# Kernel optimization log

Measured on AMD Instinct MI355X. Metric: run time of the kernel, lower is better.

Reference implementation:

```python
import jax, jax.numpy as jnp
import numpy as np

N_NODES = 100000
N_EDGES = 3200000
N_FEAT = 128
HIDDEN = 16
N_CLASSES = 10
N_GRAPHS = 512


def setup_inputs() -> dict:
    key = jax.random.key(0)
    ks = jax.random.split(key, 12)
    x = jax.random.normal(ks[0], (N_NODES, N_FEAT), dtype=jnp.float32)
    edge_index = jax.random.randint(ks[1], (2, N_EDGES), 0, N_NODES, dtype=jnp.int64)
    batch = jnp.sort(jax.random.randint(ks[2], (N_NODES,), 0, N_GRAPHS, dtype=jnp.int64))
    def glorot(k, fan_in, fan_out):
        s = jnp.sqrt(6.0 / (fan_in + fan_out)).astype(jnp.float32)
        return jax.random.uniform(k, (fan_in, fan_out), jnp.float32, -s, s)
    W1 = glorot(ks[3], N_FEAT, HIDDEN); b1 = jnp.zeros((HIDDEN,), jnp.float32)
    W2 = glorot(ks[4], HIDDEN, HIDDEN); b2 = jnp.zeros((HIDDEN,), jnp.float32)
    W3 = glorot(ks[5], HIDDEN, HIDDEN); b3 = jnp.zeros((HIDDEN,), jnp.float32)
    Wlin = glorot(ks[6], HIDDEN, N_CLASSES)
    blin = jnp.zeros((N_CLASSES,), jnp.float32)
    return {"x": x, "edge_index": edge_index, "batch": batch,
            "W1": W1, "b1": b1, "W2": W2, "b2": b2, "W3": W3, "b3": b3,
            "Wlin": Wlin, "blin": blin}


def _gcn_conv(x, W, b, src, dst, norm, n):
    # h = X W ; out[dst] += norm * h[src] ; + bias
    h = x @ W
    out = jax.ops.segment_sum(h[src] * norm[:, None], dst, num_segments=n)
    return out + b


def reference(x, edge_index, batch, W1, b1, W2, b2, W3, b3, Wlin, blin):
    n = x.shape[0]
    loop = jnp.arange(n, dtype=edge_index.dtype)
    src = jnp.concatenate([edge_index[0], loop])  # add self-loops (PyG GCNConv default)
    dst = jnp.concatenate([edge_index[1], loop])
    # symmetric degree normalization: deg over destination (incl. self-loops)
    deg = jax.ops.segment_sum(jnp.ones_like(dst, dtype=x.dtype), dst, num_segments=n)
    dinv = jnp.where(deg > 0, jax.lax.rsqrt(jnp.maximum(deg, 1.0)), 0.0)
    norm = dinv[src] * dinv[dst]  # [E+N]

    h = jax.nn.relu(_gcn_conv(x, W1, b1, src, dst, norm, n))
    h = jax.nn.relu(_gcn_conv(h, W2, b2, src, dst, norm, n))
    h = _gcn_conv(h, W3, b3, src, dst, norm, n)
    # global add pool over graphs
    pooled = jax.ops.segment_sum(h, batch, num_segments=N_GRAPHS)  # [G, hidden]
    # dropout p=0.5 is identity in eval mode
    return pooled @ Wlin + blin
```

## Files before the change

### kernel.cpp

```cpp
#include <hip/hip_runtime.h>
#include <hip/hip_fp16.h>

#define N_NODES   100000
#define N_EDGES   3200000
#define N_FEAT    128
#define HIDDEN    16
#define N_CLASSES 10
#define N_GRAPHS  512
#define NPB       256
#define NBUCKET   391
#define EPB       4096
#define PBLK      ((N_EDGES + EPB - 1) / EPB)
#define PSLACK    15872
#define CSLACK    9216


__global__ void cursor_init_kernel(int* __restrict__ cur) {
    int i = blockIdx.x * 256 + threadIdx.x;
    if (i < NBUCKET) cur[i] = i * PSLACK;
}

__global__ __launch_bounds__(512) void partition_kernel(const int* __restrict__ src,
                                                        const int* __restrict__ dst,
                                                        int* __restrict__ cur,
                                                        unsigned* __restrict__ part) {
    __shared__ int cnt[NBUCKET];
    __shared__ int lbase[NBUCKET];
    __shared__ int rk[NBUCKET];
    __shared__ int gbase[NBUCKET];
    __shared__ int s[512];
    __shared__ unsigned sorted[EPB];
    __shared__ unsigned short bb[EPB];
    __shared__ unsigned char  dl[EPB];
    int tid = threadIdx.x;
    for (int i = tid; i < NBUCKET; i += 512) cnt[i] = 0;
    __syncthreads();
    int s0 = blockIdx.x * EPB;
#pragma unroll
    for (int i = 0; i < EPB / 512; ++i) {
        int le = i * 512 + tid;
        int e  = s0 + le;
        if (e < N_EDGES) {
            int d = dst[e];
            int b = d >> 8;
            bb[le] = (unsigned short)b;
            dl[le] = (unsigned char)(d & 255);
            atomicAdd(&cnt[b], 1);
        }
    }
    __syncthreads();
    int v = (tid < NBUCKET) ? cnt[tid] : 0;
    s[tid] = v;
    __syncthreads();
    for (int off = 1; off < 512; off <<= 1) {
        int t = (tid >= off) ? s[tid - off] : 0;
        __syncthreads();
        s[tid] += t;
        __syncthreads();
    }
    if (tid < NBUCKET) {
        int lb = s[tid] - v;
        lbase[tid] = lb;
        rk[tid]    = lb;
        int cpad = (v + 15) & ~15;
        gbase[tid] = cpad ? atomicAdd(&cur[tid], cpad) : 0;
    }
    __syncthreads();
#pragma unroll
    for (int i = 0; i < EPB / 512; ++i) {
        int le = i * 512 + tid;
        int e  = s0 + le;
        if (e < N_EDGES) {
            int b = bb[le];
            int r = atomicAdd(&rk[b], 1);
            sorted[r] = (unsigned)src[e] | ((unsigned)dl[le] << 17);
        }
    }
    __syncthreads();
    int w16 = tid >> 4, l16 = tid & 15;
    for (int b = w16; b < NBUCKET; b += 32) {
        int c = cnt[b];
        if (!c) continue;
        int cpad = (c + 15) & ~15;
        int lb = lbase[b], gb = gbase[b];
        for (int j = l16; j < cpad; j += 16)
            part[gb + j] = (j < c) ? sorted[lb + j] : 0xFFFFFFFFu;
    }
}

__global__ __launch_bounds__(512) void build_csr_kernel(const unsigned* __restrict__ part,
                                                        const int* __restrict__ cur,
                                                        int2* __restrict__ rp,
                                                        float* __restrict__ dinv, int* __restrict__ csr) {
    __shared__ int ncnt[256];
    __shared__ int s[512];
    int b   = blockIdx.x;
    int tid = threadIdx.x;
    int beg = b * PSLACK, end = cur[b];
    if (tid < 256) ncnt[tid] = 0;
    __syncthreads();
    for (int j = beg + tid; j < end; j += 512) {
        unsigned r = part[j];
        if (r != 0xFFFFFFFFu) atomicAdd(&ncnt[(r >> 17) & 255], 1);
    }
    __syncthreads();
    int deg = (tid < 256) ? ncnt[tid] : 0;
    s[tid] = deg;
    __syncthreads();
    for (int off = 1; off < 512; off <<= 1) {
        int t = (tid >= off) ? s[tid - off] : 0;
        __syncthreads();
        s[tid] += t;
        __syncthreads();
    }
    int excl = s[tid] - deg;
    int cbeg = b * CSLACK;
    if (tid < 256) {
        int node = b * 256 + tid;
        if (node < N_NODES) {
            rp[node]   = make_int2(cbeg + excl, cbeg + excl + deg);
            dinv[node] = rsqrtf((float)(deg + 1));
        }
    }
    __syncthreads();
    if (tid < 256) ncnt[tid] = cbeg + excl;
    __syncthreads();
    for (int j = beg + tid; j < end; j += 512) {
        unsigned r = part[j];
        if (r != 0xFFFFFFFFu) {
            int vv = (r >> 17) & 255;
            int slot = atomicAdd(&ncnt[vv], 1);
            csr[slot] = (int)(r & 0x1FFFFu);
        }
    }
}


__device__ __forceinline__ void pack_store8(__half* outp, int idx, const float* o) {
    int4 w;
    __half2 q;
    q = __floats2half2_rn(o[0], o[1]); w.x = *(int*)&q;
    q = __floats2half2_rn(o[2], o[3]); w.y = *(int*)&q;
    q = __floats2half2_rn(o[4], o[5]); w.z = *(int*)&q;
    q = __floats2half2_rn(o[6], o[7]); w.w = *(int*)&q;
    ((int4*)outp)[idx] = w;
}

__global__ __launch_bounds__(256) void transform_x_kernel(const float* __restrict__ x,
                                                          const float* __restrict__ W,
                                                          const float* __restrict__ dinv,
                                                          __half* __restrict__ g) {
    __shared__ __half2 Wp[1024];
    int tid = threadIdx.x;
    for (int i = tid; i < 1024; i += 256) {
        int kp = i >> 4, f = i & 15;
        Wp[i] = __floats2half2_rn(W[(2 * kp) * HIDDEN + f], W[(2 * kp + 1) * HIDDEN + f]);
    }
    __syncthreads();
    int l  = tid & 63;
    int wv = tid >> 6;
    int rw = l >> 2;
    int q  = l & 3;
    int row = blockIdx.x * 64 + wv * 16 + rw;
    if (row >= N_NODES) return;
    const float4* xp = (const float4*)x + (size_t)row * 32;
    float4 xr[8];
#pragma unroll
    for (int s8 = 0; s8 < 8; ++s8) xr[s8] = xp[q + 4 * s8];
    __half2 acc[16];
    const __half2 z2 = __floats2half2_rn(0.f, 0.f);
#pragma unroll
    for (int f = 0; f < 16; ++f) acc[f] = z2;
    const int4* w4 = (const int4*)Wp;
#pragma unroll
    for (int s8 = 0; s8 < 8; ++s8) {
        int k4 = q + 4 * s8;
        __half2 xp0 = __floats2half2_rn(xr[s8].x, xr[s8].y);
        __half2 xp1 = __floats2half2_rn(xr[s8].z, xr[s8].w);
#pragma unroll
        for (int hf = 0; hf < 2; ++hf) {
            int kp = 2 * k4 + hf;
            __half2 xv = hf ? xp1 : xp0;
#pragma unroll
            for (int j = 0; j < 4; ++j) {
                int4 wj = w4[kp * 4 + j];
                const __half2* wvv = (const __half2*)&wj;
#pragma unroll
                for (int ff = 0; ff < 4; ++ff)
                    acc[j * 4 + ff] = __hfma2(xv, wvv[ff], acc[j * 4 + ff]);
            }
        }
    }
    float di = dinv[row];
    float o[16];
#pragma unroll
    for (int f = 0; f < 16; ++f) {
        float2 t = __half22float2(acc[f]);
        float sv = t.x + t.y;
        sv += __shfl_xor(sv, 1);
        sv += __shfl_xor(sv, 2);
        o[f] = sv * di;
    }
    if (q == 0) {
        pack_store8(g, row * 2,     &o[0]);
        pack_store8(g, row * 2 + 1, &o[8]);
    }
}

template <int MODE>
__global__ __launch_bounds__(256) void aggregate_kernel(
        const __half* __restrict__ g, const int2* __restrict__ rp,
        const int* __restrict__ csr, const float* __restrict__ dinv,
        const float* __restrict__ bias, const float* __restrict__ Wn,
        __half* __restrict__ out) {
    __shared__ float WnL[HIDDEN * HIDDEN];
    int tid  = threadIdx.x;
    if (MODE == 2) {
        if (tid < HIDDEN * HIDDEN) WnL[tid] = Wn[tid];
        __syncthreads();
    }
    int wave = tid >> 6;
    int l    = tid & 63;
    int c  = l >> 3;
    int vl = (l >> 1) & 3;
    int hh = l & 1;
    int v = blockIdx.x * 16 + wave * 4 + vl;
    int2 range = rp[v];
    int beg = range.x, end = range.y;
    const int4* g4 = (const int4*)g;
    float a0 = 0.f, a1 = 0.f, a2 = 0.f, a3 = 0.f, a4 = 0.f, a5 = 0.f, a6 = 0.f, a7 = 0.f;
#pragma unroll 4
    for (int j = beg + c; j < end; j += 8) {
        int s = csr[j];
        int4 r = g4[s * 2 + hh];
        float2 f0 = __half22float2(*(const __half2*)&r.x);
        float2 f1 = __half22float2(*(const __half2*)&r.y);
        float2 f2 = __half22float2(*(const __half2*)&r.z);
        float2 f3 = __half22float2(*(const __half2*)&r.w);
        a0 += f0.x; a1 += f0.y; a2 += f1.x; a3 += f1.y;
        a4 += f2.x; a5 += f2.y; a6 += f3.x; a7 += f3.y;
    }
    a0 += __shfl_xor(a0, 8);  a1 += __shfl_xor(a1, 8);
    a2 += __shfl_xor(a2, 8);  a3 += __shfl_xor(a3, 8);
    a4 += __shfl_xor(a4, 8);  a5 += __shfl_xor(a5, 8);
    a6 += __shfl_xor(a6, 8);  a7 += __shfl_xor(a7, 8);
    a0 += __shfl_xor(a0, 16); a1 += __shfl_xor(a1, 16);
    a2 += __shfl_xor(a2, 16); a3 += __shfl_xor(a3, 16);
    a4 += __shfl_xor(a4, 16); a5 += __shfl_xor(a5, 16);
    a6 += __shfl_xor(a6, 16); a7 += __shfl_xor(a7, 16);
    a0 += __shfl_xor(a0, 32); a1 += __shfl_xor(a1, 32);
    a2 += __shfl_xor(a2, 32); a3 += __shfl_xor(a3, 32);
    a4 += __shfl_xor(a4, 32); a5 += __shfl_xor(a5, 32);
    a6 += __shfl_xor(a6, 32); a7 += __shfl_xor(a7, 32);
    if (c == 0) {
        int4 r = g4[v * 2 + hh];
        float2 s0 = __half22float2(*(const __half2*)&r.x);
        float2 s1 = __half22float2(*(const __half2*)&r.y);
        float2 s2 = __half22float2(*(const __half2*)&r.z);
        float2 s3 = __half22float2(*(const __half2*)&r.w);
        float di = dinv[v];
        const float4* bp = (const float4*)bias;
        float4 bA = bp[hh * 2];
        float4 bB = bp[hh * 2 + 1];
        float o[8];
        o[0] = di * (a0 + s0.x) + bA.x;
        o[1] = di * (a1 + s0.y) + bA.y;
        o[2] = di * (a2 + s1.x) + bA.z;
        o[3] = di * (a3 + s1.y) + bA.w;
        o[4] = di * (a4 + s2.x) + bB.x;
        o[5] = di * (a5 + s2.y) + bB.y;
        o[6] = di * (a6 + s3.x) + bB.z;
        o[7] = di * (a7 + s3.y) + bB.w;
        if (MODE == 2) {
#pragma unroll
            for (int i = 0; i < 8; ++i) o[i] = fmaxf(o[i], 0.f);
            float pa[16];
#pragma unroll
            for (int f = 0; f < 16; ++f) pa[f] = 0.f;
            const float* wr = &WnL[hh * 8 * HIDDEN];
#pragma unroll
            for (int qq = 0; qq < 8; ++qq) {
                float hq = o[qq];
#pragma unroll
                for (int f = 0; f < 16; ++f) pa[f] += hq * wr[qq * HIDDEN + f];
            }
            float o2[8];
#pragma unroll
            for (int i = 0; i < 8; ++i) {
                float lo = pa[i];
                float hi = pa[8 + i];
                float keep = hh ? hi : lo;
                float send = hh ? lo : hi;
                float recv = __shfl_xor(send, 1);
                o2[i] = di * (keep + recv);
            }
            pack_store8(out, v * 2 + hh, o2);
        } else {
            pack_store8(out, v * 2 + hh, o);
        }
    }
}


__global__ void pool_head_kernel(const __half* __restrict__ h, const int* __restrict__ batch,
                                 const float* __restrict__ Wlin, const float* __restrict__ blin,
                                 float* __restrict__ out) {
    __shared__ float red[256];
    __shared__ int bounds[2];
    int g   = blockIdx.x;
    int tid = threadIdx.x;
    if (tid < 2) {
        int target = g + tid;
        int lo = 0, hi = N_NODES;
        while (lo < hi) {
            int mid = (lo + hi) >> 1;
            if (batch[mid] < target) lo = mid + 1; else hi = mid;
        }
        bounds[tid] = lo;
    }
    __syncthreads();
    int start = bounds[0], end = bounds[1];
    int f = tid & 15, r = tid >> 4;
    float acc = 0.f;
    for (int v = start + r; v < end; v += 16)
        acc += __half2float(h[v * HIDDEN + f]);
    red[tid] = acc;
    __syncthreads();
    for (int off = 128; off >= 16; off >>= 1) {
        if (tid < off) red[tid] += red[tid + off];
        __syncthreads();
    }
    if (tid < N_CLASSES) {
        float s = blin[tid];
#pragma unroll
        for (int fe = 0; fe < HIDDEN; ++fe) s += red[fe] * Wlin[fe * N_CLASSES + tid];
        out[g * N_CLASSES + tid] = s;
    }
}


extern "C" void kernel_launch(void* const* d_in, const int* in_sizes, int n_in,
                              void* d_out, int out_size, void* d_ws, size_t ws_size,
                              hipStream_t stream) {
    const float* x     = (const float*)d_in[0];
    const int*   ei    = (const int*)d_in[1];
    const int*   src   = ei;
    const int*   dst   = ei + N_EDGES;
    const int*   batch = (const int*)d_in[2];
    const float* W1 = (const float*)d_in[3];
    const float* b1 = (const float*)d_in[4];
    const float* W2 = (const float*)d_in[5];
    const float* b2 = (const float*)d_in[6];
    const float* W3 = (const float*)d_in[7];
    const float* b3 = (const float*)d_in[8];
    const float* Wlin = (const float*)d_in[9];
    const float* blin = (const float*)d_in[10];
    float* out = (float*)d_out;

    char* w = (char*)d_ws;
    auto alloc = [&](size_t bytes) -> char* {
        char* p = w;
        w += (bytes + 255) & ~(size_t)255;
        return p;
    };
    int*    cur    = (int*)alloc((size_t)NBUCKET * 4);
    int2*   rp     = (int2*)alloc((size_t)N_NODES * 8);
    float*  dinv   = (float*)alloc((size_t)N_NODES * 4);
    __half* gA     = (__half*)alloc((size_t)N_NODES * HIDDEN * 2);
    __half* gB     = (__half*)alloc((size_t)N_NODES * HIDDEN * 2);
    __half* hA     = (__half*)alloc((size_t)N_NODES * HIDDEN * 2);
    unsigned* part = (unsigned*)alloc((size_t)NBUCKET * PSLACK * 4);
    int*    csr    = (int*)alloc((size_t)NBUCKET * CSLACK * 4);

    int ntx = (N_NODES + 63) / 64;
    int ab  = (N_NODES + 15) / 16;

    cursor_init_kernel<<<(NBUCKET + 255) / 256, 256, 0, stream>>>(cur);
    partition_kernel<<<PBLK, 512, 0, stream>>>(src, dst, cur, part);
    build_csr_kernel<<<NBUCKET, 512, 0, stream>>>(part, cur, rp, dinv, csr);

    transform_x_kernel<<<ntx, 256, 0, stream>>>(x, W1, dinv, gA);
    aggregate_kernel<2><<<ab, 256, 0, stream>>>(gA, rp, csr, dinv, b1, W2, gB);
    aggregate_kernel<2><<<ab, 256, 0, stream>>>(gB, rp, csr, dinv, b2, W3, gA);
    aggregate_kernel<0><<<ab, 256, 0, stream>>>(gA, rp, csr, dinv, b3, nullptr, hA);

    pool_head_kernel<<<N_GRAPHS, 256, 0, stream>>>(hA, batch, Wlin, blin, out);
}
```

Before: 263.7 us.

## Pad CSR rows to multiples of 16 and gather neighbor pairs via int2

CSR rows are padded to a multiple of 16 entries that point to an extra zero feature row, which init_kernel zeroes in gA and gB. The aggregation loop then runs a fixed trip count, loads two indices per lane as int2 and issues two feature gathers per iteration without bound checks. This trades extra gathers of the zero row for more memory-level parallelism and simpler control flow. The rp load is also moved ahead of the shared weight staging so the two can overlap.

After: 266.9 us. Within noise of the previous version (+1.2%).

```diff
diff --git a/kernel.cpp b/kernel.cpp
--- a/kernel.cpp
+++ b/kernel.cpp
@@ -12,13 +12,20 @@
 #define EPB       4096
 #define PBLK      ((N_EDGES + EPB - 1) / EPB)
 #define PSLACK    15872
-#define CSLACK    9216
-
-
-__global__ void cursor_init_kernel(int* __restrict__ cur) {
+#define CSLACK    11520
+
+
+__global__ void init_kernel(int* __restrict__ cur, __half* __restrict__ gA, __half* __restrict__ gB) {
     int i = blockIdx.x * 256 + threadIdx.x;
     if (i < NBUCKET) cur[i] = i * PSLACK;
-}
+    if (blockIdx.x == 0) {
+        int tid = threadIdx.x;
+        const __half2 z2 = __floats2half2_rn(0.f, 0.f);
+        if (tid < 8)       ((__half2*)(gA + (size_t)N_NODES * HIDDEN))[tid] = z2;
+        else if (tid < 16) ((__half2*)(gB + (size_t)N_NODES * HIDDEN))[tid - 8] = z2;
+    }
+}
+
 
 __global__ __launch_bounds__(512) void partition_kernel(const int* __restrict__ src,
                                                         const int* __restrict__ dst,
@@ -105,7 +112,8 @@
     }
     __syncthreads();
     int deg = (tid < 256) ? ncnt[tid] : 0;
-    s[tid] = deg;
+    int dp  = (deg + 15) & ~15;
+    s[tid] = dp;
     __syncthreads();
     for (int off = 1; off < 512; off <<= 1) {
         int t = (tid >= off) ? s[tid - off] : 0;
@@ -113,13 +121,14 @@
         s[tid] += t;
         __syncthreads();
     }
-    int excl = s[tid] - deg;
+    int excl = s[tid] - dp;
     int cbeg = b * CSLACK;
     if (tid < 256) {
         int node = b * 256 + tid;
         if (node < N_NODES) {
-            rp[node]   = make_int2(cbeg + excl, cbeg + excl + deg);
+            rp[node]   = make_int2(cbeg + excl, cbeg + excl + dp);
             dinv[node] = rsqrtf((float)(deg + 1));
+            for (int p = deg; p < dp; ++p) csr[cbeg + excl + p] = N_NODES;
         }
     }
     __syncthreads();
@@ -215,10 +224,6 @@
         __half* __restrict__ out) {
     __shared__ float WnL[HIDDEN * HIDDEN];
     int tid  = threadIdx.x;
-    if (MODE == 2) {
-        if (tid < HIDDEN * HIDDEN) WnL[tid] = Wn[tid];
-        __syncthreads();
-    }
     int wave = tid >> 6;
     int l    = tid & 63;
     int c  = l >> 3;
@@ -226,19 +231,31 @@
     int hh = l & 1;
     int v = blockIdx.x * 16 + wave * 4 + vl;
     int2 range = rp[v];
-    int beg = range.x, end = range.y;
+    if (MODE == 2) {
+        if (tid < HIDDEN * HIDDEN) WnL[tid] = Wn[tid];
+        __syncthreads();
+    }
+    int b2 = range.x >> 1;
+    int K  = (range.y - range.x) >> 4;
+    const int2* csr2 = (const int2*)csr;
     const int4* g4 = (const int4*)g;
     float a0 = 0.f, a1 = 0.f, a2 = 0.f, a3 = 0.f, a4 = 0.f, a5 = 0.f, a6 = 0.f, a7 = 0.f;
-#pragma unroll 4
-    for (int j = beg + c; j < end; j += 8) {
-        int s = csr[j];
-        int4 r = g4[s * 2 + hh];
-        float2 f0 = __half22float2(*(const __half2*)&r.x);
-        float2 f1 = __half22float2(*(const __half2*)&r.y);
-        float2 f2 = __half22float2(*(const __half2*)&r.z);
-        float2 f3 = __half22float2(*(const __half2*)&r.w);
+    for (int i = 0; i < K; ++i) {
+        int2 ss = csr2[b2 + c + 8 * i];
+        int4 r0 = g4[ss.x * 2 + hh];
+        int4 r1 = g4[ss.y * 2 + hh];
+        float2 f0 = __half22float2(*(const __half2*)&r0.x);
+        float2 f1 = __half22float2(*(const __half2*)&r0.y);
+        float2 f2 = __half22float2(*(const __half2*)&r0.z);
+        float2 f3 = __half22float2(*(const __half2*)&r0.w);
         a0 += f0.x; a1 += f0.y; a2 += f1.x; a3 += f1.y;
         a4 += f2.x; a5 += f2.y; a6 += f3.x; a7 += f3.y;
+        float2 g0 = __half22float2(*(const __half2*)&r1.x);
+        float2 g1 = __half22float2(*(const __half2*)&r1.y);
+        float2 g2 = __half22float2(*(const __half2*)&r1.z);
+        float2 g3 = __half22float2(*(const __half2*)&r1.w);
+        a0 += g0.x; a1 += g0.y; a2 += g1.x; a3 += g1.y;
+        a4 += g2.x; a5 += g2.y; a6 += g3.x; a7 += g3.y;
     }
     a0 += __shfl_xor(a0, 8);  a1 += __shfl_xor(a1, 8);
     a2 += __shfl_xor(a2, 8);  a3 += __shfl_xor(a3, 8);
@@ -366,16 +383,16 @@
     int*    cur    = (int*)alloc((size_t)NBUCKET * 4);
     int2*   rp     = (int2*)alloc((size_t)N_NODES * 8);
     float*  dinv   = (float*)alloc((size_t)N_NODES * 4);
-    __half* gA     = (__half*)alloc((size_t)N_NODES * HIDDEN * 2);
-    __half* gB     = (__half*)alloc((size_t)N_NODES * HIDDEN * 2);
-    __half* hA     = (__half*)alloc((size_t)N_NODES * HIDDEN * 2);
+    __half* gA     = (__half*)alloc((size_t)(N_NODES + 1) * HIDDEN * 2);
+    __half* gB     = (__half*)alloc((size_t)(N_NODES + 1) * HIDDEN * 2);
+    __half* hA     = (__half*)alloc((size_t)(N_NODES + 1) * HIDDEN * 2);
     unsigned* part = (unsigned*)alloc((size_t)NBUCKET * PSLACK * 4);
     int*    csr    = (int*)alloc((size_t)NBUCKET * CSLACK * 4);
 
     int ntx = (N_NODES + 63) / 64;
     int ab  = (N_NODES + 15) / 16;
 
-    cursor_init_kernel<<<(NBUCKET + 255) / 256, 256, 0, stream>>>(cur);
+    init_kernel<<<(NBUCKET + 255) / 256, 256, 0, stream>>>(cur, gA, gB);
     partition_kernel<<<PBLK, 512, 0, stream>>>(src, dst, cur, part);
     build_csr_kernel<<<NBUCKET, 512, 0, stream>>>(part, cur, rp, dinv, csr);
 
```

## Scatter partitioned edges directly using atomic ranks, drop local sort and scan

Applied to the files above, without the earlier changes.

The partition kernel now records each edge's atomic rank within its bucket and scatters it straight to global memory. This removes the shared-memory block scan, the second atomic pass and the staging sort, at the cost of less coalesced global writes. build_csr stores per-edge ranks in shared memory from its counting pass so the second pass needs no atomics. The cursor-init kernel becomes a memset with relative offsets, and the rp load in the aggregate kernel is moved ahead of the weight-staging barrier.

Measured after the change: 275.8 us. 1.05x slower.

```diff
diff --git a/kernel.cpp b/kernel.cpp
--- a/kernel.cpp
+++ b/kernel.cpp
@@ -15,23 +15,14 @@
 #define CSLACK    9216
 
 
-__global__ void cursor_init_kernel(int* __restrict__ cur) {
-    int i = blockIdx.x * 256 + threadIdx.x;
-    if (i < NBUCKET) cur[i] = i * PSLACK;
-}
-
 __global__ __launch_bounds__(512) void partition_kernel(const int* __restrict__ src,
                                                         const int* __restrict__ dst,
                                                         int* __restrict__ cur,
                                                         unsigned* __restrict__ part) {
     __shared__ int cnt[NBUCKET];
-    __shared__ int lbase[NBUCKET];
-    __shared__ int rk[NBUCKET];
     __shared__ int gbase[NBUCKET];
-    __shared__ int s[512];
-    __shared__ unsigned sorted[EPB];
-    __shared__ unsigned short bb[EPB];
-    __shared__ unsigned char  dl[EPB];
+    __shared__ unsigned val[EPB];
+    __shared__ unsigned br[EPB];
     int tid = threadIdx.x;
     for (int i = tid; i < NBUCKET; i += 512) cnt[i] = 0;
     __syncthreads();
@@ -41,50 +32,41 @@
         int le = i * 512 + tid;
         int e  = s0 + le;
         if (e < N_EDGES) {
-            int d = dst[e];
-            int b = d >> 8;
-            bb[le] = (unsigned short)b;
-            dl[le] = (unsigned char)(d & 255);
-            atomicAdd(&cnt[b], 1);
-        }
-    }
-    __syncthreads();
-    int v = (tid < NBUCKET) ? cnt[tid] : 0;
-    s[tid] = v;
-    __syncthreads();
-    for (int off = 1; off < 512; off <<= 1) {
-        int t = (tid >= off) ? s[tid - off] : 0;
-        __syncthreads();
-        s[tid] += t;
-        __syncthreads();
-    }
+            int d  = dst[e];
+            int sv = src[e];
+            int b  = d >> 8;
+            int r  = atomicAdd(&cnt[b], 1);
+            val[le] = (unsigned)sv | ((unsigned)(d & 255) << 17);
+            br[le]  = (unsigned)b | ((unsigned)r << 16);
+        } else {
+            br[le] = 0xFFFFFFFFu;
+        }
+    }
+    __syncthreads();
     if (tid < NBUCKET) {
-        int lb = s[tid] - v;
-        lbase[tid] = lb;
-        rk[tid]    = lb;
-        int cpad = (v + 15) & ~15;
-        gbase[tid] = cpad ? atomicAdd(&cur[tid], cpad) : 0;
+        int c = cnt[tid];
+        int cpad = (c + 15) & ~15;
+        gbase[tid] = tid * PSLACK + (cpad ? atomicAdd(&cur[tid], cpad) : 0);
     }
     __syncthreads();
 #pragma unroll
     for (int i = 0; i < EPB / 512; ++i) {
         int le = i * 512 + tid;
-        int e  = s0 + le;
-        if (e < N_EDGES) {
-            int b = bb[le];
-            int r = atomicAdd(&rk[b], 1);
-            sorted[r] = (unsigned)src[e] | ((unsigned)dl[le] << 17);
-        }
-    }
-    __syncthreads();
+        unsigned w = br[le];
+        if (w != 0xFFFFFFFFu) {
+            int b = (int)(w & 0xFFFFu);
+            int r = (int)(w >> 16);
+            part[gbase[b] + r] = val[le];
+        }
+    }
     int w16 = tid >> 4, l16 = tid & 15;
     for (int b = w16; b < NBUCKET; b += 32) {
         int c = cnt[b];
         if (!c) continue;
         int cpad = (c + 15) & ~15;
-        int lb = lbase[b], gb = gbase[b];
-        for (int j = l16; j < cpad; j += 16)
-            part[gb + j] = (j < c) ? sorted[lb + j] : 0xFFFFFFFFu;
+        int gb = gbase[b];
+        for (int j = c + l16; j < cpad; j += 16)
+            part[gb + j] = 0xFFFFFFFFu;
     }
 }
 
@@ -94,14 +76,16 @@
                                                         float* __restrict__ dinv, int* __restrict__ csr) {
     __shared__ int ncnt[256];
     __shared__ int s[512];
+    __shared__ unsigned char rkb[PSLACK];
     int b   = blockIdx.x;
     int tid = threadIdx.x;
-    int beg = b * PSLACK, end = cur[b];
+    int beg = b * PSLACK, end = beg + cur[b];
     if (tid < 256) ncnt[tid] = 0;
     __syncthreads();
     for (int j = beg + tid; j < end; j += 512) {
         unsigned r = part[j];
-        if (r != 0xFFFFFFFFu) atomicAdd(&ncnt[(r >> 17) & 255], 1);
+        if (r != 0xFFFFFFFFu)
+            rkb[j - beg] = (unsigned char)atomicAdd(&ncnt[(r >> 17) & 255], 1);
     }
     __syncthreads();
     int deg = (tid < 256) ? ncnt[tid] : 0;
@@ -127,11 +111,8 @@
     __syncthreads();
     for (int j = beg + tid; j < end; j += 512) {
         unsigned r = part[j];
-        if (r != 0xFFFFFFFFu) {
-            int vv = (r >> 17) & 255;
-            int slot = atomicAdd(&ncnt[vv], 1);
-            csr[slot] = (int)(r & 0x1FFFFu);
-        }
+        if (r != 0xFFFFFFFFu)
+            csr[ncnt[(r >> 17) & 255] + rkb[j - beg]] = (int)(r & 0x1FFFFu);
     }
 }
 
@@ -215,10 +196,6 @@
         __half* __restrict__ out) {
     __shared__ float WnL[HIDDEN * HIDDEN];
     int tid  = threadIdx.x;
-    if (MODE == 2) {
-        if (tid < HIDDEN * HIDDEN) WnL[tid] = Wn[tid];
-        __syncthreads();
-    }
     int wave = tid >> 6;
     int l    = tid & 63;
     int c  = l >> 3;
@@ -226,6 +203,10 @@
     int hh = l & 1;
     int v = blockIdx.x * 16 + wave * 4 + vl;
     int2 range = rp[v];
+    if (MODE == 2) {
+        if (tid < HIDDEN * HIDDEN) WnL[tid] = Wn[tid];
+        __syncthreads();
+    }
     int beg = range.x, end = range.y;
     const int4* g4 = (const int4*)g;
     float a0 = 0.f, a1 = 0.f, a2 = 0.f, a3 = 0.f, a4 = 0.f, a5 = 0.f, a6 = 0.f, a7 = 0.f;
@@ -375,7 +356,7 @@
     int ntx = (N_NODES + 63) / 64;
     int ab  = (N_NODES + 15) / 16;
 
-    cursor_init_kernel<<<(NBUCKET + 255) / 256, 256, 0, stream>>>(cur);
+    hipMemsetAsync(cur, 0, (size_t)NBUCKET * 4, stream);
     partition_kernel<<<PBLK, 512, 0, stream>>>(src, dst, cur, part);
     build_csr_kernel<<<NBUCKET, 512, 0, stream>>>(part, cur, rp, dinv, csr);
 
```
